# Performance work log

Measured on AMD Instinct MI355X. Metric: run time of the kernel, lower is better.

Reference implementation:

```python
import jax, jax.numpy as jnp
import numpy as np

T, D, H, E, K = 4096, 1024, 2048, 8, 2  # tokens, input_size, hidden_size, num_experts, top_k


def setup_inputs() -> dict:
    key = jax.random.key(0)
    k1, k2, k3, k4, k5 = jax.random.split(key, 5)
    x = jax.random.normal(k1, (T, D), dtype=jnp.float32)
    expert_p = jax.random.uniform(k2, (T, K), dtype=jnp.float32)
    expert_idxs = jax.random.randint(k3, (T, K), 0, E, dtype=jnp.int32).astype(jnp.int64)
    # ParallelExperts weights: up-proj D -> 2H (h | gates), down-proj H -> D
    W_up = jax.random.normal(k4, (E, D, 2 * H), dtype=jnp.float32) * (D ** -0.5)
    W_down = jax.random.normal(k5, (E, H, D), dtype=jnp.float32) * (H ** -0.5)
    return {"x": x, "expert_p": expert_p, "expert_idxs": expert_idxs, "W_up": W_up, "W_down": W_down}


def reference(x, expert_p, expert_idxs, W_up, W_down):
    # x: [T, D]; expert_p/expert_idxs: [T, K]; W_up: [E, D, 2H]; W_down: [E, H, D]
    t = x.shape[0]
    e = W_up.shape[0]
    # Up projection for every expert, then GLU: out = silu(gates) * h with (h, gates) = chunk(up, 2)
    up = jnp.einsum('td,edh->teh', x, W_up)                  # [T, E, 2H]
    h, gates = jnp.split(up, 2, axis=-1)                     # each [T, E, H]
    act = jax.nn.silu(gates) * h                             # [T, E, H]
    y_all = jnp.einsum('teh,ehd->ted', act, W_down)          # [T, E, D]
    # Scatter gating weights to dense [T, E] (equivalent to sparse combine over top-k)
    dense_g = jnp.zeros((t, e), dtype=x.dtype).at[
        jnp.arange(t)[:, None], expert_idxs].add(expert_p)   # [T, E]
    y = jnp.einsum('ted,te->td', y_all, dense_g)             # [T, D]
    return y
```

## Files before the change

kernel.cpp:

```cpp
#include <hip/hip_runtime.h>
#include <hip/hip_bf16.h>
#include <stdint.h>

#define TT    4096
#define DD    1024
#define HH    2048
#define TWOH  4096
#define EE    8
#define NPAIR 8192

typedef __attribute__((ext_vector_type(8))) short bf16x8;
typedef __attribute__((ext_vector_type(4))) float f32x4;

__device__ __forceinline__ unsigned short f32_bf16(float f) {
  union { float f; unsigned int u; } v; v.f = f;
  return (unsigned short)((v.u + 0x7FFFu + ((v.u >> 16) & 1u)) >> 16);
}

__device__ __forceinline__ void gload_lds16(const unsigned short* g, unsigned short* l) {
  __builtin_amdgcn_global_load_lds(
      (const __attribute__((address_space(1))) unsigned int*)g,
      (__attribute__((address_space(3))) unsigned int*)l, 16, 0, 0);
}

__global__ void k_convert_x(const float* __restrict__ x, unsigned short* __restrict__ xb) {
  int i = blockIdx.x * blockDim.x + threadIdx.x;
  const float4* x4 = (const float4*)x;
  float4 v = x4[i];
  ushort4 o;
  o.x = f32_bf16(v.x); o.y = f32_bf16(v.y); o.z = f32_bf16(v.z); o.w = f32_bf16(v.w);
  *(ushort4*)(xb + (size_t)i * 4) = o;
}

__global__ void k_transpose_bf16(const float* __restrict__ src, unsigned short* __restrict__ dst,
                                 int R, int C) {
  __shared__ float tile[32][33];
  int e = blockIdx.z;
  const float* s = src + (size_t)e * R * C;
  unsigned short* d = dst + (size_t)e * R * C;
  int c0 = blockIdx.x * 32, r0 = blockIdx.y * 32;
  int tx = threadIdx.x, ty = threadIdx.y;
#pragma unroll
  for (int i = 0; i < 32; i += 8)
    tile[ty + i][tx] = s[(size_t)(r0 + ty + i) * C + c0 + tx];
  __syncthreads();
#pragma unroll
  for (int i = 0; i < 32; i += 8)
    d[(size_t)(c0 + ty + i) * R + r0 + tx] = f32_bf16(tile[tx][ty + i]);
}

__global__ void k_route(const int* __restrict__ idx, const float* __restrict__ p,
                        int* __restrict__ tok, float* __restrict__ pw, int* __restrict__ se) {
  __shared__ int cnt[EE];
  __shared__ int base[EE];
  __shared__ int cur[EE];
  int t = threadIdx.x;
  if (t < EE) cnt[t] = 0;
  __syncthreads();
  for (int i = t; i < NPAIR; i += blockDim.x) atomicAdd(&cnt[idx[i]], 1);
  __syncthreads();
  if (t == 0) {
    int acc = 0;
    for (int e = 0; e < EE; e++) { base[e] = acc; cur[e] = acc; acc += cnt[e]; }
  }
  __syncthreads();
  for (int i = t; i < NPAIR; i += blockDim.x) {
    int e = idx[i];
    int pos = atomicAdd(&cur[e], 1);
    tok[pos] = i >> 1;
    pw[pos]  = p[i];
  }
  if (t < EE) { se[t] = base[t]; se[EE + t] = base[t] + cnt[t]; }
}

__launch_bounds__(256)
__global__ void k_gemm1(const unsigned short* __restrict__ xb,
                        const unsigned short* __restrict__ wup,
                        const int* __restrict__ tok,
                        const int* __restrict__ se,
                        unsigned short* __restrict__ act) {
  const int e = blockIdx.z;
  const int start = se[e], end = se[EE + e];
  const int row_base = start + blockIdx.y * 128;
  if (row_base >= end) return;
  const int c0 = blockIdx.x * 64;

  __shared__ __align__(16) unsigned short Als[128 * 64];
  __shared__ __align__(16) unsigned short Bls[128 * 64];

  const int t = threadIdx.x;
  const int lane = t & 63;
  const int w = t >> 6;
  const int wr = w >> 1, wc = w & 1;

  const int srow = t >> 3;
  const int ls = (t & 7) ^ (srow & 7);
  const unsigned short* wup_e = wup + (size_t)e * TWOH * DD;

  const unsigned short* srcA[4];
  const unsigned short* srcB[4];
  unsigned short* dstA[4];
  unsigned short* dstB[4];
#pragma unroll
  for (int i = 0; i < 4; i++) {
    int row = i * 32 + srow;
    int ridx = row_base + row; if (ridx > end - 1) ridx = end - 1;
    srcA[i] = xb + (size_t)tok[ridx] * DD + ls * 8;
    int nrow = (row < 64) ? (c0 + row) : (HH + c0 + (row - 64));
    srcB[i] = wup_e + (size_t)nrow * DD + ls * 8;
    dstA[i] = Als + ((size_t)i * 256 + t) * 8;
    dstB[i] = Bls + ((size_t)i * 256 + t) * 8;
  }

  f32x4 acc_h[4][2], acc_g[4][2];
#pragma unroll
  for (int m = 0; m < 4; m++)
#pragma unroll
    for (int n = 0; n < 2; n++) {
      acc_h[m][n] = (f32x4){0.f, 0.f, 0.f, 0.f};
      acc_g[m][n] = (f32x4){0.f, 0.f, 0.f, 0.f};
    }

  for (int kt = 0; kt < DD / 64; kt++) {
#pragma unroll
    for (int i = 0; i < 4; i++) gload_lds16(srcA[i], dstA[i]);
#pragma unroll
    for (int i = 0; i < 4; i++) gload_lds16(srcB[i], dstB[i]);
#pragma unroll
    for (int i = 0; i < 4; i++) { srcA[i] += 64; srcB[i] += 64; }
    __syncthreads();

#pragma unroll
    for (int ksub = 0; ksub < 2; ksub++) {
      const int kslot = ksub * 4 + (lane >> 4);
      bf16x8 a[4], bh[2], bg[2];
#pragma unroll
      for (int m = 0; m < 4; m++) {
        int r = wr * 64 + m * 16 + (lane & 15);
        a[m] = *(const bf16x8*)(Als + r * 64 + ((kslot ^ (r & 7)) * 8));
      }
#pragma unroll
      for (int n = 0; n < 2; n++) {
        int rh = wc * 32 + n * 16 + (lane & 15);
        bh[n] = *(const bf16x8*)(Bls + rh * 64 + ((kslot ^ (rh & 7)) * 8));
        int rg = 64 + rh;
        bg[n] = *(const bf16x8*)(Bls + rg * 64 + ((kslot ^ (rg & 7)) * 8));
      }
#pragma unroll
      for (int m = 0; m < 4; m++)
#pragma unroll
        for (int n = 0; n < 2; n++) {
          acc_h[m][n] = __builtin_amdgcn_mfma_f32_16x16x32_bf16(a[m], bh[n], acc_h[m][n], 0, 0, 0);
          acc_g[m][n] = __builtin_amdgcn_mfma_f32_16x16x32_bf16(a[m], bg[n], acc_g[m][n], 0, 0, 0);
        }
    }
    __syncthreads();
  }

#pragma unroll
  for (int m = 0; m < 4; m++) {
#pragma unroll
    for (int j = 0; j < 4; j++) {
      int rloc = wr * 64 + m * 16 + ((lane >> 4) * 4) + j;
      int rg = row_base + rloc;
      if (rg < end) {
#pragma unroll
        for (int n = 0; n < 2; n++) {
          float h = acc_h[m][n][j];
          float g = acc_g[m][n][j];
          float sv = (g / (1.f + __expf(-g))) * h;
          act[(size_t)rg * HH + (c0 + wc * 32 + n * 16 + (lane & 15))] = f32_bf16(sv);
        }
      }
    }
  }
}

__launch_bounds__(256)
__global__ void k_gemm2(const unsigned short* __restrict__ act,
                        const unsigned short* __restrict__ wdn,
                        const int* __restrict__ tok,
                        const float* __restrict__ pw,
                        const int* __restrict__ se,
                        float* __restrict__ y) {
  const int e = blockIdx.z;
  const int start = se[e], end = se[EE + e];
  const int row_base = start + blockIdx.y * 128;
  if (row_base >= end) return;
  const int c0 = blockIdx.x * 128;

  __shared__ __align__(16) unsigned short Als[128 * 64];
  __shared__ __align__(16) unsigned short Bls[128 * 64];

  const int t = threadIdx.x;
  const int lane = t & 63;
  const int w = t >> 6;
  const int wr = w >> 1, wc = w & 1;

  const int srow = t >> 3;
  const int ls = (t & 7) ^ (srow & 7);
  const unsigned short* wdn_e = wdn + (size_t)e * DD * HH;

  const unsigned short* srcA[4];
  const unsigned short* srcB[4];
  unsigned short* dstA[4];
  unsigned short* dstB[4];
#pragma unroll
  for (int i = 0; i < 4; i++) {
    int row = i * 32 + srow;
    int ridx = row_base + row; if (ridx > end - 1) ridx = end - 1;
    srcA[i] = act + (size_t)ridx * HH + ls * 8;
    srcB[i] = wdn_e + (size_t)(c0 + row) * HH + ls * 8;
    dstA[i] = Als + ((size_t)i * 256 + t) * 8;
    dstB[i] = Bls + ((size_t)i * 256 + t) * 8;
  }

  f32x4 acc[4][4];
#pragma unroll
  for (int m = 0; m < 4; m++)
#pragma unroll
    for (int n = 0; n < 4; n++) acc[m][n] = (f32x4){0.f, 0.f, 0.f, 0.f};

  for (int kt = 0; kt < HH / 64; kt++) {
#pragma unroll
    for (int i = 0; i < 4; i++) gload_lds16(srcA[i], dstA[i]);
#pragma unroll
    for (int i = 0; i < 4; i++) gload_lds16(srcB[i], dstB[i]);
#pragma unroll
    for (int i = 0; i < 4; i++) { srcA[i] += 64; srcB[i] += 64; }
    __syncthreads();

#pragma unroll
    for (int ksub = 0; ksub < 2; ksub++) {
      const int kslot = ksub * 4 + (lane >> 4);
      bf16x8 a[4], b[4];
#pragma unroll
      for (int m = 0; m < 4; m++) {
        int r = wr * 64 + m * 16 + (lane & 15);
        a[m] = *(const bf16x8*)(Als + r * 64 + ((kslot ^ (r & 7)) * 8));
      }
#pragma unroll
      for (int n = 0; n < 4; n++) {
        int rb = wc * 64 + n * 16 + (lane & 15);
        b[n] = *(const bf16x8*)(Bls + rb * 64 + ((kslot ^ (rb & 7)) * 8));
      }
#pragma unroll
      for (int m = 0; m < 4; m++)
#pragma unroll
        for (int n = 0; n < 4; n++)
          acc[m][n] = __builtin_amdgcn_mfma_f32_16x16x32_bf16(a[m], b[n], acc[m][n], 0, 0, 0);
    }
    __syncthreads();
  }

#pragma unroll
  for (int m = 0; m < 4; m++) {
#pragma unroll
    for (int j = 0; j < 4; j++) {
      int rloc = wr * 64 + m * 16 + ((lane >> 4) * 4) + j;
      int rg = row_base + rloc;
      if (rg < end) {
        int tk = tok[rg];
        float p = pw[rg];
#pragma unroll
        for (int n = 0; n < 4; n++) {
          int col = c0 + wc * 64 + n * 16 + (lane & 15);
          atomicAdd(&y[(size_t)tk * DD + col], p * acc[m][n][j]);
        }
      }
    }
  }
}

extern "C" void kernel_launch(void* const* d_in, const int* in_sizes, int n_in,
                              void* d_out, int out_size, void* d_ws, size_t ws_size,
                              hipStream_t stream) {
  const float* x        = (const float*)d_in[0];
  const float* expert_p = (const float*)d_in[1];
  const int*   expert_i = (const int*)d_in[2];
  const float* W_up     = (const float*)d_in[3];
  const float* W_down   = (const float*)d_in[4];
  float* y = (float*)d_out;

  char* ws = (char*)d_ws;
  const size_t OFF_XB  = 0;
  const size_t OFF_WUP = 8388608;
  const size_t OFF_WDN = 75497472;
  const size_t OFF_ACT = 109051904;
  const size_t OFF_TOK = 142606336;
  const size_t OFF_PW  = 142639104;
  const size_t OFF_SE  = 142671872;

  unsigned short* xb   = (unsigned short*)(ws + OFF_XB);
  unsigned short* wupb = (unsigned short*)(ws + OFF_WUP);
  unsigned short* wdnb = (unsigned short*)(ws + OFF_WDN);
  unsigned short* actb = (unsigned short*)(ws + OFF_ACT);
  int*   tok = (int*)(ws + OFF_TOK);
  float* pw  = (float*)(ws + OFF_PW);
  int*   se  = (int*)(ws + OFF_SE);

  k_convert_x<<<(TT * DD / 4 + 255) / 256, 256, 0, stream>>>(x, xb);
  k_transpose_bf16<<<dim3(TWOH / 32, DD / 32, EE), dim3(32, 8), 0, stream>>>(W_up, wupb, DD, TWOH);
  k_transpose_bf16<<<dim3(DD / 32, HH / 32, EE), dim3(32, 8), 0, stream>>>(W_down, wdnb, HH, DD);
  k_route<<<1, 1024, 0, stream>>>(expert_i, expert_p, tok, pw, se);
  k_gemm1<<<dim3(HH / 64, NPAIR / 128, EE), 256, 0, stream>>>(xb, wupb, tok, se, actb);
  hipMemsetAsync(d_out, 0, (size_t)TT * DD * sizeof(float), stream);
  k_gemm2<<<dim3(DD / 128, NPAIR / 128, EE), 256, 0, stream>>>(actb, wdnb, tok, pw, se, y);
}
```

Measured before the change: 494.8 us.

## Replace atomic scatter with per-pair writes plus gather combine; vectorize weight transpose

gemm2 now stores each routed pair's weighted output row into a scratch buffer instead of atomically adding into y. A new combine kernel gathers each token's two rows through an inverse-permutation array that the routing kernel records. This removes the output memset and the float atomics, at the cost of an extra 32MB write and read of scratch, which reuses the no-longer-needed up-weight region. Separately, the weight transpose/convert kernel uses 64x64 tiles with float4 loads and 4-wide bf16 stores to improve memory efficiency.

```diff
diff --git a/kernel.cpp b/kernel.cpp
--- a/kernel.cpp
+++ b/kernel.cpp
@@ -32,25 +32,41 @@
   *(ushort4*)(xb + (size_t)i * 4) = o;
 }
 
-__global__ void k_transpose_bf16(const float* __restrict__ src, unsigned short* __restrict__ dst,
-                                 int R, int C) {
-  __shared__ float tile[32][33];
+__global__ void k_transpose64(const float* __restrict__ src, unsigned short* __restrict__ dst,
+                              int R, int C) {
+  __shared__ float tile[64][65];
   int e = blockIdx.z;
   const float* s = src + (size_t)e * R * C;
   unsigned short* d = dst + (size_t)e * R * C;
-  int c0 = blockIdx.x * 32, r0 = blockIdx.y * 32;
-  int tx = threadIdx.x, ty = threadIdx.y;
-#pragma unroll
-  for (int i = 0; i < 32; i += 8)
-    tile[ty + i][tx] = s[(size_t)(r0 + ty + i) * C + c0 + tx];
+  int c0 = blockIdx.x * 64, r0 = blockIdx.y * 64;
+  int t = threadIdx.x;
+  int lr = t >> 4;
+  int lc = (t & 15) * 4;
+#pragma unroll
+  for (int i = 0; i < 4; i++) {
+    int r = i * 16 + lr;
+    float4 v = *(const float4*)(s + (size_t)(r0 + r) * C + c0 + lc);
+    tile[r][lc + 0] = v.x; tile[r][lc + 1] = v.y;
+    tile[r][lc + 2] = v.z; tile[r][lc + 3] = v.w;
+  }
   __syncthreads();
-#pragma unroll
-  for (int i = 0; i < 32; i += 8)
-    d[(size_t)(c0 + ty + i) * R + r0 + tx] = f32_bf16(tile[tx][ty + i]);
+  int sc = t >> 4;
+  int sr = (t & 15) * 4;
+#pragma unroll
+  for (int i = 0; i < 4; i++) {
+    int c = i * 16 + sc;
+    ushort4 o;
+    o.x = f32_bf16(tile[sr + 0][c]);
+    o.y = f32_bf16(tile[sr + 1][c]);
+    o.z = f32_bf16(tile[sr + 2][c]);
+    o.w = f32_bf16(tile[sr + 3][c]);
+    *(ushort4*)(d + (size_t)(c0 + c) * R + r0 + sr) = o;
+  }
 }
 
 __global__ void k_route(const int* __restrict__ idx, const float* __restrict__ p,
-                        int* __restrict__ tok, float* __restrict__ pw, int* __restrict__ se) {
+                        int* __restrict__ tok, float* __restrict__ pw,
+                        int* __restrict__ inv, int* __restrict__ se) {
   __shared__ int cnt[EE];
   __shared__ int base[EE];
   __shared__ int cur[EE];
@@ -69,6 +85,7 @@
     int pos = atomicAdd(&cur[e], 1);
     tok[pos] = i >> 1;
     pw[pos]  = p[i];
+    inv[i]   = pos;
   }
   if (t < EE) { se[t] = base[t]; se[EE + t] = base[t] + cnt[t]; }
 }
@@ -179,10 +196,9 @@
 __launch_bounds__(256)
 __global__ void k_gemm2(const unsigned short* __restrict__ act,
                         const unsigned short* __restrict__ wdn,
-                        const int* __restrict__ tok,
                         const float* __restrict__ pw,
                         const int* __restrict__ se,
-                        float* __restrict__ y) {
+                        float* __restrict__ yp) {
   const int e = blockIdx.z;
   const int start = se[e], end = se[EE + e];
   const int row_base = start + blockIdx.y * 128;
@@ -260,16 +276,27 @@
       int rloc = wr * 64 + m * 16 + ((lane >> 4) * 4) + j;
       int rg = row_base + rloc;
       if (rg < end) {
-        int tk = tok[rg];
         float p = pw[rg];
 #pragma unroll
         for (int n = 0; n < 4; n++) {
           int col = c0 + wc * 64 + n * 16 + (lane & 15);
-          atomicAdd(&y[(size_t)tk * DD + col], p * acc[m][n][j]);
+          yp[(size_t)rg * DD + col] = p * acc[m][n][j];
         }
       }
     }
   }
+}
+
+__global__ void k_combine(const float* __restrict__ yp, const int* __restrict__ inv,
+                          float* __restrict__ y) {
+  int i = blockIdx.x * blockDim.x + threadIdx.x;
+  int tk = i >> 8;
+  int d4 = i & 255;
+  const float4* yp4 = (const float4*)yp;
+  float4 a = yp4[(size_t)inv[2 * tk] * (DD / 4) + d4];
+  float4 b = yp4[(size_t)inv[2 * tk + 1] * (DD / 4) + d4];
+  float4 o = make_float4(a.x + b.x, a.y + b.y, a.z + b.z, a.w + b.w);
+  ((float4*)y)[i] = o;
 }
 
 extern "C" void kernel_launch(void* const* d_in, const int* in_sizes, int n_in,
@@ -289,21 +316,24 @@
   const size_t OFF_ACT = 109051904;
   const size_t OFF_TOK = 142606336;
   const size_t OFF_PW  = 142639104;
-  const size_t OFF_SE  = 142671872;
+  const size_t OFF_INV = 142671872;
+  const size_t OFF_SE  = 142704640;
 
   unsigned short* xb   = (unsigned short*)(ws + OFF_XB);
   unsigned short* wupb = (unsigned short*)(ws + OFF_WUP);
   unsigned short* wdnb = (unsigned short*)(ws + OFF_WDN);
   unsigned short* actb = (unsigned short*)(ws + OFF_ACT);
+  float* yp  = (float*)(ws + OFF_WUP);
   int*   tok = (int*)(ws + OFF_TOK);
   float* pw  = (float*)(ws + OFF_PW);
+  int*   inv = (int*)(ws + OFF_INV);
   int*   se  = (int*)(ws + OFF_SE);
 
   k_convert_x<<<(TT * DD / 4 + 255) / 256, 256, 0, stream>>>(x, xb);
-  k_transpose_bf16<<<dim3(TWOH / 32, DD / 32, EE), dim3(32, 8), 0, stream>>>(W_up, wupb, DD, TWOH);
-  k_transpose_bf16<<<dim3(DD / 32, HH / 32, EE), dim3(32, 8), 0, stream>>>(W_down, wdnb, HH, DD);
-  k_route<<<1, 1024, 0, stream>>>(expert_i, expert_p, tok, pw, se);
+  k_transpose64<<<dim3(TWOH / 64, DD / 64, EE), 256, 0, stream>>>(W_up, wupb, DD, TWOH);
+  k_transpose64<<<dim3(DD / 64, HH / 64, EE), 256, 0, stream>>>(W_down, wdnb, HH, DD);
+  k_route<<<1, 1024, 0, stream>>>(expert_i, expert_p, tok, pw, inv, se);
   k_gemm1<<<dim3(HH / 64, NPAIR / 128, EE), 256, 0, stream>>>(xb, wupb, tok, se, actb);
-  hipMemsetAsync(d_out, 0, (size_t)TT * DD * sizeof(float), stream);
-  k_gemm2<<<dim3(DD / 128, NPAIR / 128, EE), 256, 0, stream>>>(actb, wdnb, tok, pw, se, y);
-}
+  k_gemm2<<<dim3(DD / 128, NPAIR / 128, EE), 256, 0, stream>>>(actb, wdnb, pw, se, yp);
+  k_combine<<<(TT * DD / 4) / 256, 256, 0, stream>>>(yp, inv, y);
+}
```

New measurement: 471.6 us. 1.05x faster.
